# Kernel tuning notes

Hardware: AMD Instinct MI355X
Metric: run time of the kernel (lower is better)

Reference implementation:

```python
import jax, jax.numpy as jnp
import numpy as np


def setup_inputs() -> dict:
    key = jax.random.key(0)
    k1, k2 = jax.random.split(key)
    B, S, D, K = 16, 4096, 256, 4096
    x = jax.random.normal(k1, (B, S, D), dtype=jnp.float32)
    scale = 1.0 / K  # matches nn.init.uniform_(-scale, scale)
    embeddings = jax.random.uniform(k2, (K, D), dtype=jnp.float32, minval=-scale, maxval=scale)
    return {"x": x, "embeddings": embeddings}


def reference(x, embeddings):
    # Flatten all leading dims: [N, D]
    in_shape = x.shape
    flat = x.reshape(-1, in_shape[-1])
    distances = (
        jnp.sum(flat ** 2, axis=1, keepdims=True)
        + jnp.sum(embeddings ** 2, axis=1)
        - 2.0 * flat @ embeddings.T
    )
    proposal = jnp.argmin(distances, axis=-1).reshape(in_shape[:-1])  # [B, S] int
    quantized = embeddings[proposal]  # [B, S, D] gather
    return quantized, proposal
```

## Files before the change

### kernel.cpp

```cpp
#include <hip/hip_runtime.h>
#include <hip/hip_bf16.h>
#include <stdint.h>

#define NROWS 65536
#define DDIM  256
#define KCAND 4096
#define CAP   48
#define MARGIN1 8e-4f
#define MARGIN2 8e-4f

#define LSTRIDE 132
#define ROWS_PB 128

typedef __bf16 bf16x8 __attribute__((ext_vector_type(8)));
typedef float  f32x4  __attribute__((ext_vector_type(4)));
typedef unsigned int u32;
typedef unsigned long long u64;

__device__ __forceinline__ u32 f2bf_u(float f) {
    u32 u = __float_as_uint(f);
    u += 0x7fffu + ((u >> 16) & 1u);
    return u >> 16;
}
__device__ __forceinline__ u32 pack2(float lo, float hi) { return f2bf_u(lo) | (f2bf_u(hi) << 16); }
__device__ __forceinline__ u32 fkey(float f) {
    u32 u = __float_as_uint(f);
    return (u & 0x80000000u) ? ~u : (u | 0x80000000u);
}
__device__ __forceinline__ float funkey(u32 k) {
    u32 u = (k & 0x80000000u) ? (k ^ 0x80000000u) : ~k;
    return __uint_as_float(u);
}
__device__ __forceinline__ float vmax4(f32x4 v) {
    return fmaxf(fmaxf(v[0], v[1]), fmaxf(v[2], v[3]));
}

__device__ __forceinline__ float exact_r(const float* __restrict__ xr, float A,
                                         const float* __restrict__ er) {
    float b = 0.f, acc = 0.f;
    #pragma unroll 8
    for (int d = 0; d < DDIM; ++d) {
        float e = er[d];
        b   = fmaf(e, e, b);
        acc = fmaf(2.0f * xr[d], e, acc);
    }
    return (A + b) - acc;
}

__launch_bounds__(256)
__global__ void convert_e(const float* __restrict__ e, u32* __restrict__ ebf) {
    int T = blockIdx.x * blockDim.x + threadIdx.x;
    int L = T & 63, u = (T >> 6) & 3, kc = (T >> 8) & 7, s = T >> 11;
    int cand = s * 64 + u * 16 + (L & 15);
    int k0 = kc * 32 + (L >> 4) * 8;
    const float4* src = (const float4*)(e + (size_t)cand * DDIM + k0);
    float4 a = src[0], b = src[1];
    uint4 o;
    o.x = pack2(a.x, a.y); o.y = pack2(a.z, a.w);
    o.z = pack2(b.x, b.y); o.w = pack2(b.z, b.w);
    ((uint4*)ebf)[T] = o;
}

__launch_bounds__(256, 2)
__global__ void phase1(const float* __restrict__ x, const u32* __restrict__ ebf,
                       u32* __restrict__ cnt, uint2* __restrict__ list) {
    __shared__ u32 lxd[ROWS_PB * LSTRIDE];
    __shared__ u32 rowBestK[ROWS_PB];

    const int tid = threadIdx.x;
    const int rowBase = blockIdx.x * ROWS_PB;
    if (tid < ROWS_PB) rowBestK[tid] = 0x007FFFFFu;

    {
        const float4* x4 = (const float4*)(x + (size_t)rowBase * DDIM);
        #pragma unroll
        for (int j = 0; j < 32; ++j) {
            int idx = j * 256 + tid;
            int r = idx >> 6, c4 = idx & 63;
            float4 v = x4[idx];
            *(uint2*)&lxd[r * LSTRIDE + 2 * c4] = make_uint2(pack2(v.x, v.y), pack2(v.z, v.w));
        }
    }
    __syncthreads();

    const int L = tid & 63;
    const int w = __builtin_amdgcn_readfirstlane(tid >> 6);
    const int lq = L >> 4, ln = L & 15;
    const int vL = L << 4;

    const char* ebc_w = (const char*)ebf + (size_t)w * 32768;

    auto loadB = [&](int it_, int kc_, bf16x8* dst) {
        const char* kb = ebc_w + (size_t)it_ * 131072 + kc_ * 4096;
        #pragma unroll
        for (int u = 0; u < 4; ++u)
            dst[u] = *(const bf16x8*)(kb + u * 1024 + vL);
    };

    const char* pa = (const char*)lxd + ln * (LSTRIDE * 4) + lq * 16;

    bf16x8 bb[2][4];
    f32x4 acc[8][4];
    const f32x4 Z4 = {0.f, 0.f, 0.f, 0.f};

    loadB(0, 0, bb[0]);
    #pragma unroll
    for (int kc = 0; kc < 8; ++kc) {
        if (kc < 7) loadB(0, kc + 1, bb[(kc + 1) & 1]);
        #pragma unroll
        for (int a = 0; a < 8; ++a) {
            bf16x8 fa = *(const bf16x8*)(pa + a * (16 * LSTRIDE * 4) + kc * 64);
            #pragma unroll
            for (int u = 0; u < 4; ++u)
                acc[a][u] = (kc == 0)
                    ? __builtin_amdgcn_mfma_f32_16x16x32_bf16(bb[0][u], fa, Z4, 0, 0, 0)
                    : __builtin_amdgcn_mfma_f32_16x16x32_bf16(bb[kc & 1][u], fa, acc[a][u], 0, 0, 0);
        }
    }
    #pragma unroll
    for (int a = 0; a < 8; ++a) {
        float lmax = fmaxf(fmaxf(vmax4(acc[a][0]), vmax4(acc[a][1])),
                           fmaxf(vmax4(acc[a][2]), vmax4(acc[a][3])));
        float m = fmaxf(lmax, __shfl_xor(lmax, 16, 64));
        m = fmaxf(m, __shfl_xor(m, 32, 64));
        if (lq == 0) atomicMax(&rowBestK[a * 16 + ln], fkey(m));
    }
    __syncthreads();

    loadB(0, 0, bb[0]);
    #pragma unroll 1
    for (int it = 0; it < 16; ++it) {
        {
            loadB(it, 1, bb[1]);
            #pragma unroll
            for (int a = 0; a < 8; ++a) {
                bf16x8 fa = *(const bf16x8*)(pa + a * (16 * LSTRIDE * 4));
                #pragma unroll
                for (int u = 0; u < 4; ++u)
                    acc[a][u] = __builtin_amdgcn_mfma_f32_16x16x32_bf16(bb[0][u], fa, Z4, 0, 0, 0);
            }
        }
        #pragma unroll
        for (int kc = 1; kc < 8; ++kc) {
            int g = it * 8 + kc;
            if (g < 127) { int gn = g + 1; loadB(gn >> 3, gn & 7, bb[(kc + 1) & 1]); }
            #pragma unroll
            for (int a = 0; a < 8; ++a) {
                bf16x8 fa = *(const bf16x8*)(pa + a * (16 * LSTRIDE * 4) + kc * 64);
                #pragma unroll
                for (int u = 0; u < 4; ++u)
                    acc[a][u] = __builtin_amdgcn_mfma_f32_16x16x32_bf16(bb[kc & 1][u], fa, acc[a][u], 0, 0, 0);
            }
        }

        int strip = it * 4 + w;
        u32 seen[8];
        #pragma unroll
        for (int a = 0; a < 8; ++a) seen[a] = rowBestK[a * 16 + ln];

        #pragma unroll
        for (int a = 0; a < 8; ++a) {
            float lmax = fmaxf(fmaxf(vmax4(acc[a][0]), vmax4(acc[a][1])),
                               fmaxf(vmax4(acc[a][2]), vmax4(acc[a][3])));
            float m = fmaxf(lmax, __shfl_xor(lmax, 16, 64));
            m = fmaxf(m, __shfl_xor(m, 32, 64));
            if (lq == 0) atomicMax(&rowBestK[a * 16 + ln], fkey(m));
            float eff  = fmaxf(m, funkey(seen[a]));
            float thrA = eff - 0.5f * MARGIN1;
            if (__ballot(lmax >= thrA)) {
                int c = 0;
                #pragma unroll
                for (int u = 0; u < 4; ++u)
                    #pragma unroll
                    for (int r = 0; r < 4; ++r)
                        c += (acc[a][u][r] >= thrA) ? 1 : 0;
                int p = c, t;
                t = __shfl_up(p, 16, 64); if (lq >= 1) p += t;
                t = __shfl_up(p, 32, 64); if (lq >= 2) p += t;
                int grow = rowBase + a * 16 + ln;
                u32 base = 0;
                if (lq == 3 && p > 0) base = atomicAdd(&cnt[grow], (u32)p);
                base = __shfl(base, 48 + ln, 64);
                u32 pos = base + (u32)(p - c);
                #pragma unroll
                for (int u = 0; u < 4; ++u)
                    #pragma unroll
                    for (int r = 0; r < 4; ++r) {
                        float av = acc[a][u][r];
                        if (av >= thrA) {
                            if (pos < CAP)
                                list[(size_t)grow * CAP + pos] =
                                    make_uint2(__float_as_uint(-2.f * av),
                                               (u32)(strip * 64 + u * 16 + lq * 4 + r));
                            ++pos;
                        }
                    }
            }
        }
    }
}

__launch_bounds__(256)
__global__ void phase2(const float* __restrict__ x, const float* __restrict__ emb,
                       const u32* __restrict__ cnt, const uint2* __restrict__ list,
                       float* __restrict__ outq, float* __restrict__ outp) {
    __shared__ float xs[4][DDIM];
    const int wid = threadIdx.x >> 6;
    const int row = blockIdx.x * 4 + wid;
    const int L   = threadIdx.x & 63;

    u32 n = cnt[row];
    u32 kstar;

    if (n == 1) {
        kstar = list[(size_t)row * CAP].y;
    } else {
        bool scan_all = (n > CAP);
        bool resolved = false;
        float vv = INFINITY; u32 kk = 0;
        bool surv = false;
        if (!scan_all) {
            if (L < (int)n) { uint2 e = list[(size_t)row * CAP + L]; vv = __uint_as_float(e.x); kk = e.y; }
            float mv = vv;
            #pragma unroll
            for (int o = 32; o; o >>= 1) mv = fminf(mv, __shfl_xor(mv, o, 64));
            surv = (L < (int)n) && (vv <= mv + MARGIN2);
            u64 bal = __ballot(surv);
            if (__popcll(bal) == 1) {
                kstar = __shfl(kk, (int)(__ffsll(bal) - 1), 64);
                resolved = true;
            }
        }
        if (!resolved) {
            float4 v = ((const float4*)(x + (size_t)row * DDIM))[L];
            *(float4*)&xs[wid][L * 4] = v;
            double s = (double)v.x * v.x + (double)v.y * v.y + (double)v.z * v.z + (double)v.w * v.w;
            #pragma unroll
            for (int o = 32; o; o >>= 1) s += __shfl_xor(s, o, 64);
            float A = (float)s;

            u64 key = 0xFFFFFFFFFFFFFFFFull;
            if (!scan_all) {
                if (surv) {
                    float r = exact_r(xs[wid], A, emb + (size_t)kk * DDIM);
                    key = ((u64)fkey(r) << 32) | (u64)kk;
                }
            } else {
                for (int c = 0; c < KCAND / 64; ++c) {
                    u32 k = (u32)(c * 64 + L);
                    float r = exact_r(xs[wid], A, emb + (size_t)k * DDIM);
                    u64 cand = ((u64)fkey(r) << 32) | (u64)k;
                    key = (cand < key) ? cand : key;
                }
            }
            #pragma unroll
            for (int o = 32; o; o >>= 1) {
                u64 other = __shfl_xor(key, o, 64);
                key = (other < key) ? other : key;
            }
            kstar = (u32)(key & 0xFFFFFFFFull);
        }
    }

    float4 q = ((const float4*)(emb + (size_t)kstar * DDIM))[L];
    ((float4*)(outq + (size_t)row * DDIM))[L] = q;
    if (L == 0) outp[row] = (float)kstar;
}

extern "C" void kernel_launch(void* const* d_in, const int* in_sizes, int n_in,
                              void* d_out, int out_size, void* d_ws, size_t ws_size,
                              hipStream_t stream) {
    const float* x   = (const float*)d_in[0];
    const float* emb = (const float*)d_in[1];
    float* outq = (float*)d_out;
    float* outp = outq + (size_t)NROWS * DDIM;

    char* ws = (char*)d_ws;
    u32*   ebf  = (u32*)ws;
    u32*   cnt  = (u32*)(ws + (2u << 20));
    uint2* list = (uint2*)(ws + (3u << 20));

    hipMemsetAsync(cnt, 0, (size_t)NROWS * sizeof(u32), stream);
    convert_e<<<512, 256, 0, stream>>>(emb, ebf);
    phase1<<<NROWS / ROWS_PB, 256, 0, stream>>>(x, ebf, cnt, list);
    phase2<<<NROWS / 4, 256, 0, stream>>>(x, emb, cnt, list, outq, outp);
}
```

Baseline: 396.2 us.

## Halve per-wave candidate tile and deepen embedding prefetch to a 4-slot ring

Each wave now processes 32 codebook candidates per iteration instead of 64, over twice as many iterations. The accumulator tile shrinks from 8x4 to 8x2 MFMA blocks, and B-fragment loads are prefetched two steps ahead through a 4-entry register ring. The aim is to cut VGPR pressure, which may raise occupancy, and to hide global load latency better. The cost is that each LDS A-fragment read now feeds only two MFMAs instead of four, so LDS traffic per unit of work doubles and the loop overhead grows.

Measured after the change: 454.7 us. +14.7%, slower.

```diff
diff --git a/kernel.cpp b/kernel.cpp
--- a/kernel.cpp
+++ b/kernel.cpp
@@ -88,68 +88,81 @@
     const int lq = L >> 4, ln = L & 15;
     const int vL = L << 4;
 
-    const char* ebc_w = (const char*)ebf + (size_t)w * 32768;
-
-    auto loadB = [&](int it_, int kc_, bf16x8* dst) {
-        const char* kb = ebc_w + (size_t)it_ * 131072 + kc_ * 4096;
-        #pragma unroll
-        for (int u = 0; u < 4; ++u)
+    const char* ebc_w2 = (const char*)ebf + (w >> 1) * 32768 + (w & 1) * 2048;
+
+    auto loadG = [&](int it_, int kc_, bf16x8* dst) {
+        const char* kb = ebc_w2 + (size_t)it_ * 65536 + kc_ * 4096;
+        #pragma unroll
+        for (int u = 0; u < 2; ++u)
             dst[u] = *(const bf16x8*)(kb + u * 1024 + vL);
     };
 
     const char* pa = (const char*)lxd + ln * (LSTRIDE * 4) + lq * 16;
 
-    bf16x8 bb[2][4];
-    f32x4 acc[8][4];
+    bf16x8 bbr[4][2];
+    f32x4 acc[8][2];
     const f32x4 Z4 = {0.f, 0.f, 0.f, 0.f};
 
-    loadB(0, 0, bb[0]);
-    #pragma unroll
-    for (int kc = 0; kc < 8; ++kc) {
-        if (kc < 7) loadB(0, kc + 1, bb[(kc + 1) & 1]);
+    loadG(0, 0, bbr[0]);
+    loadG(0, 1, bbr[1]);
+    #pragma unroll 1
+    for (int pit = 0; pit < 2; ++pit) {
+        #pragma unroll
+        for (int kc = 0; kc < 8; ++kc) {
+            int g = pit * 8 + kc;
+            if (g + 2 < 16) {
+                int itp = pit + (kc >= 6 ? 1 : 0);
+                loadG(itp, (kc + 2) & 7, bbr[(kc + 2) & 3]);
+            }
+            #pragma unroll
+            for (int h = 0; h < 2; ++h) {
+                bf16x8 fa[4];
+                #pragma unroll
+                for (int t = 0; t < 4; ++t)
+                    fa[t] = *(const bf16x8*)(pa + (h * 4 + t) * (16 * LSTRIDE * 4) + kc * 64);
+                #pragma unroll
+                for (int t = 0; t < 4; ++t)
+                    #pragma unroll
+                    for (int u = 0; u < 2; ++u)
+                        acc[h * 4 + t][u] = (kc == 0)
+                            ? __builtin_amdgcn_mfma_f32_16x16x32_bf16(bbr[0][u], fa[t], Z4, 0, 0, 0)
+                            : __builtin_amdgcn_mfma_f32_16x16x32_bf16(bbr[kc & 3][u], fa[t], acc[h * 4 + t][u], 0, 0, 0);
+            }
+        }
         #pragma unroll
         for (int a = 0; a < 8; ++a) {
-            bf16x8 fa = *(const bf16x8*)(pa + a * (16 * LSTRIDE * 4) + kc * 64);
-            #pragma unroll
-            for (int u = 0; u < 4; ++u)
-                acc[a][u] = (kc == 0)
-                    ? __builtin_amdgcn_mfma_f32_16x16x32_bf16(bb[0][u], fa, Z4, 0, 0, 0)
-                    : __builtin_amdgcn_mfma_f32_16x16x32_bf16(bb[kc & 1][u], fa, acc[a][u], 0, 0, 0);
-        }
-    }
-    #pragma unroll
-    for (int a = 0; a < 8; ++a) {
-        float lmax = fmaxf(fmaxf(vmax4(acc[a][0]), vmax4(acc[a][1])),
-                           fmaxf(vmax4(acc[a][2]), vmax4(acc[a][3])));
-        float m = fmaxf(lmax, __shfl_xor(lmax, 16, 64));
-        m = fmaxf(m, __shfl_xor(m, 32, 64));
-        if (lq == 0) atomicMax(&rowBestK[a * 16 + ln], fkey(m));
+            float lmax = fmaxf(vmax4(acc[a][0]), vmax4(acc[a][1]));
+            float m = fmaxf(lmax, __shfl_xor(lmax, 16, 64));
+            m = fmaxf(m, __shfl_xor(m, 32, 64));
+            if (lq == 0) atomicMax(&rowBestK[a * 16 + ln], fkey(m));
+        }
     }
     __syncthreads();
 
-    loadB(0, 0, bb[0]);
+    loadG(0, 0, bbr[0]);
+    loadG(0, 1, bbr[1]);
     #pragma unroll 1
-    for (int it = 0; it < 16; ++it) {
-        {
-            loadB(it, 1, bb[1]);
-            #pragma unroll
-            for (int a = 0; a < 8; ++a) {
-                bf16x8 fa = *(const bf16x8*)(pa + a * (16 * LSTRIDE * 4));
-                #pragma unroll
-                for (int u = 0; u < 4; ++u)
-                    acc[a][u] = __builtin_amdgcn_mfma_f32_16x16x32_bf16(bb[0][u], fa, Z4, 0, 0, 0);
-            }
-        }
-        #pragma unroll
-        for (int kc = 1; kc < 8; ++kc) {
+    for (int it = 0; it < 32; ++it) {
+        #pragma unroll
+        for (int kc = 0; kc < 8; ++kc) {
             int g = it * 8 + kc;
-            if (g < 127) { int gn = g + 1; loadB(gn >> 3, gn & 7, bb[(kc + 1) & 1]); }
-            #pragma unroll
-            for (int a = 0; a < 8; ++a) {
-                bf16x8 fa = *(const bf16x8*)(pa + a * (16 * LSTRIDE * 4) + kc * 64);
-                #pragma unroll
-                for (int u = 0; u < 4; ++u)
-                    acc[a][u] = __builtin_amdgcn_mfma_f32_16x16x32_bf16(bb[kc & 1][u], fa, acc[a][u], 0, 0, 0);
+            if (g + 2 < 256) {
+                int itp = it + (kc >= 6 ? 1 : 0);
+                loadG(itp, (kc + 2) & 7, bbr[(kc + 2) & 3]);
+            }
+            #pragma unroll
+            for (int h = 0; h < 2; ++h) {
+                bf16x8 fa[4];
+                #pragma unroll
+                for (int t = 0; t < 4; ++t)
+                    fa[t] = *(const bf16x8*)(pa + (h * 4 + t) * (16 * LSTRIDE * 4) + kc * 64);
+                #pragma unroll
+                for (int t = 0; t < 4; ++t)
+                    #pragma unroll
+                    for (int u = 0; u < 2; ++u)
+                        acc[h * 4 + t][u] = (kc == 0)
+                            ? __builtin_amdgcn_mfma_f32_16x16x32_bf16(bbr[0][u], fa[t], Z4, 0, 0, 0)
+                            : __builtin_amdgcn_mfma_f32_16x16x32_bf16(bbr[kc & 3][u], fa[t], acc[h * 4 + t][u], 0, 0, 0);
             }
         }
 
@@ -160,8 +173,7 @@
 
         #pragma unroll
         for (int a = 0; a < 8; ++a) {
-            float lmax = fmaxf(fmaxf(vmax4(acc[a][0]), vmax4(acc[a][1])),
-                               fmaxf(vmax4(acc[a][2]), vmax4(acc[a][3])));
+            float lmax = fmaxf(vmax4(acc[a][0]), vmax4(acc[a][1]));
             float m = fmaxf(lmax, __shfl_xor(lmax, 16, 64));
             m = fmaxf(m, __shfl_xor(m, 32, 64));
             if (lq == 0) atomicMax(&rowBestK[a * 16 + ln], fkey(m));
@@ -170,7 +182,7 @@
             if (__ballot(lmax >= thrA)) {
                 int c = 0;
                 #pragma unroll
-                for (int u = 0; u < 4; ++u)
+                for (int u = 0; u < 2; ++u)
                     #pragma unroll
                     for (int r = 0; r < 4; ++r)
                         c += (acc[a][u][r] >= thrA) ? 1 : 0;
@@ -183,7 +195,7 @@
                 base = __shfl(base, 48 + ln, 64);
                 u32 pos = base + (u32)(p - c);
                 #pragma unroll
-                for (int u = 0; u < 4; ++u)
+                for (int u = 0; u < 2; ++u)
                     #pragma unroll
                     for (int r = 0; r < 4; ++r) {
                         float av = acc[a][u][r];
@@ -191,7 +203,7 @@
                             if (pos < CAP)
                                 list[(size_t)grow * CAP + pos] =
                                     make_uint2(__float_as_uint(-2.f * av),
-                                               (u32)(strip * 64 + u * 16 + lq * 4 + r));
+                                               (u32)(strip * 32 + u * 16 + lq * 4 + r));
                             ++pos;
                         }
                     }
```

## Resolve unambiguous rows in phase1 epilogue and make phase2 a persistent fallback

Applied to the files above, without the earlier changes.

Moves the easy-case argmin resolution (single candidate, or a single survivor within the margin) and the codebook gather into the end of phase1, writing outputs directly and zeroing cnt for resolved rows. Phase2 becomes a grid-strided kernel of 1024 blocks that skips rows with cnt==0 and only does exact fp32 rescoring for ambiguous rows. This is meant to cut phase2's launch and per-row work for the common case. In exchange phase1 gains an extra barrier and a serial epilogue of 32 rows per wave, which reads back cnt/list from global memory.

After: 504.6 us. 27.4% more time.

```diff
diff --git a/kernel.cpp b/kernel.cpp
--- a/kernel.cpp
+++ b/kernel.cpp
@@ -63,7 +63,9 @@
 
 __launch_bounds__(256, 2)
 __global__ void phase1(const float* __restrict__ x, const u32* __restrict__ ebf,
-                       u32* __restrict__ cnt, uint2* __restrict__ list) {
+                       const float* __restrict__ emb,
+                       u32* __restrict__ cnt, uint2* __restrict__ list,
+                       float* __restrict__ outq, float* __restrict__ outp) {
     __shared__ u32 lxd[ROWS_PB * LSTRIDE];
     __shared__ u32 rowBestK[ROWS_PB];
 
@@ -198,6 +200,36 @@
             }
         }
     }
+
+    __syncthreads();
+
+    for (int rr = 0; rr < 32; ++rr) {
+        int grow = rowBase + w * 32 + rr;
+        u32 n = cnt[grow];
+        u32 kstar = 0;
+        bool resolved = false;
+        if (n == 1) {
+            kstar = list[(size_t)grow * CAP].y;
+            resolved = true;
+        } else if (n <= CAP) {
+            float vv = INFINITY; u32 kk = 0;
+            if (L < (int)n) { uint2 e = list[(size_t)grow * CAP + L]; vv = __uint_as_float(e.x); kk = e.y; }
+            float mv = vv;
+            #pragma unroll
+            for (int o = 32; o; o >>= 1) mv = fminf(mv, __shfl_xor(mv, o, 64));
+            bool surv = (L < (int)n) && (vv <= mv + MARGIN2);
+            u64 bal = __ballot(surv);
+            if (__popcll(bal) == 1) {
+                kstar = __shfl(kk, (int)(__ffsll(bal) - 1), 64);
+                resolved = true;
+            }
+        }
+        if (resolved) {
+            float4 q = ((const float4*)(emb + (size_t)kstar * DDIM))[L];
+            ((float4*)(outq + (size_t)grow * DDIM))[L] = q;
+            if (L == 0) { outp[grow] = (float)kstar; cnt[grow] = 0; }
+        }
+    }
 }
 
 __launch_bounds__(256)
@@ -206,65 +238,50 @@
                        float* __restrict__ outq, float* __restrict__ outp) {
     __shared__ float xs[4][DDIM];
     const int wid = threadIdx.x >> 6;
-    const int row = blockIdx.x * 4 + wid;
     const int L   = threadIdx.x & 63;
-
-    u32 n = cnt[row];
-    u32 kstar;
-
-    if (n == 1) {
-        kstar = list[(size_t)row * CAP].y;
-    } else {
-        bool scan_all = (n > CAP);
-        bool resolved = false;
-        float vv = INFINITY; u32 kk = 0;
-        bool surv = false;
-        if (!scan_all) {
+    const int wave0 = blockIdx.x * 4 + wid;
+
+    for (int row = wave0; row < NROWS; row += 4096) {
+        u32 n = cnt[row];
+        if (n == 0) continue;
+
+        float4 v = ((const float4*)(x + (size_t)row * DDIM))[L];
+        *(float4*)&xs[wid][L * 4] = v;
+        double s = (double)v.x * v.x + (double)v.y * v.y + (double)v.z * v.z + (double)v.w * v.w;
+        #pragma unroll
+        for (int o = 32; o; o >>= 1) s += __shfl_xor(s, o, 64);
+        float A = (float)s;
+
+        u64 key = 0xFFFFFFFFFFFFFFFFull;
+        if (n <= CAP) {
+            float vv = INFINITY; u32 kk = 0;
             if (L < (int)n) { uint2 e = list[(size_t)row * CAP + L]; vv = __uint_as_float(e.x); kk = e.y; }
             float mv = vv;
             #pragma unroll
             for (int o = 32; o; o >>= 1) mv = fminf(mv, __shfl_xor(mv, o, 64));
-            surv = (L < (int)n) && (vv <= mv + MARGIN2);
-            u64 bal = __ballot(surv);
-            if (__popcll(bal) == 1) {
-                kstar = __shfl(kk, (int)(__ffsll(bal) - 1), 64);
-                resolved = true;
-            }
-        }
-        if (!resolved) {
-            float4 v = ((const float4*)(x + (size_t)row * DDIM))[L];
-            *(float4*)&xs[wid][L * 4] = v;
-            double s = (double)v.x * v.x + (double)v.y * v.y + (double)v.z * v.z + (double)v.w * v.w;
-            #pragma unroll
-            for (int o = 32; o; o >>= 1) s += __shfl_xor(s, o, 64);
-            float A = (float)s;
-
-            u64 key = 0xFFFFFFFFFFFFFFFFull;
-            if (!scan_all) {
-                if (surv) {
-                    float r = exact_r(xs[wid], A, emb + (size_t)kk * DDIM);
-                    key = ((u64)fkey(r) << 32) | (u64)kk;
-                }
-            } else {
-                for (int c = 0; c < KCAND / 64; ++c) {
-                    u32 k = (u32)(c * 64 + L);
-                    float r = exact_r(xs[wid], A, emb + (size_t)k * DDIM);
-                    u64 cand = ((u64)fkey(r) << 32) | (u64)k;
-                    key = (cand < key) ? cand : key;
-                }
-            }
-            #pragma unroll
-            for (int o = 32; o; o >>= 1) {
-                u64 other = __shfl_xor(key, o, 64);
-                key = (other < key) ? other : key;
-            }
-            kstar = (u32)(key & 0xFFFFFFFFull);
-        }
-    }
-
-    float4 q = ((const float4*)(emb + (size_t)kstar * DDIM))[L];
-    ((float4*)(outq + (size_t)row * DDIM))[L] = q;
-    if (L == 0) outp[row] = (float)kstar;
+            if (L < (int)n && vv <= mv + MARGIN2) {
+                float r = exact_r(xs[wid], A, emb + (size_t)kk * DDIM);
+                key = ((u64)fkey(r) << 32) | (u64)kk;
+            }
+        } else {
+            for (int c = 0; c < KCAND / 64; ++c) {
+                u32 k = (u32)(c * 64 + L);
+                float r = exact_r(xs[wid], A, emb + (size_t)k * DDIM);
+                u64 cand = ((u64)fkey(r) << 32) | (u64)k;
+                key = (cand < key) ? cand : key;
+            }
+        }
+        #pragma unroll
+        for (int o = 32; o; o >>= 1) {
+            u64 other = __shfl_xor(key, o, 64);
+            key = (other < key) ? other : key;
+        }
+        u32 kstar = (u32)(key & 0xFFFFFFFFull);
+
+        float4 q = ((const float4*)(emb + (size_t)kstar * DDIM))[L];
+        ((float4*)(outq + (size_t)row * DDIM))[L] = q;
+        if (L == 0) outp[row] = (float)kstar;
+    }
 }
 
 extern "C" void kernel_launch(void* const* d_in, const int* in_sizes, int n_in,
@@ -282,6 +299,6 @@
 
     hipMemsetAsync(cnt, 0, (size_t)NROWS * sizeof(u32), stream);
     convert_e<<<512, 256, 0, stream>>>(emb, ebf);
-    phase1<<<NROWS / ROWS_PB, 256, 0, stream>>>(x, ebf, cnt, list);
-    phase2<<<NROWS / 4, 256, 0, stream>>>(x, emb, cnt, list, outq, outp);
-}
+    phase1<<<NROWS / ROWS_PB, 256, 0, stream>>>(x, ebf, emb, cnt, list, outq, outp);
+    phase2<<<1024, 256, 0, stream>>>(x, emb, cnt, list, outq, outp);
+}
```
